# Kernel tuning notes

Hardware: AMD Instinct MI355X
Metric: run time of the kernel (lower is better)

Reference implementation:

```python
import jax, jax.numpy as jnp
import numpy as np
import math

N_HEAD = 4
NORM_GROUPS = 32
EPS = 1e-5


def setup_inputs() -> dict:
    key = jax.random.key(0)
    ks = jax.random.split(key, 6)
    C = 256
    x = jax.random.normal(ks[0], (2, C, 64, 64), dtype=jnp.float32)
    gn_w = jnp.ones((C,), dtype=jnp.float32)
    gn_b = jnp.zeros((C,), dtype=jnp.float32)
    s = 1.0 / math.sqrt(C)
    wq = jax.random.normal(ks[1], (C, C), dtype=jnp.float32) * s
    wk = jax.random.normal(ks[2], (C, C), dtype=jnp.float32) * s
    wv = jax.random.normal(ks[3], (C, C), dtype=jnp.float32) * s
    wo = jax.random.normal(ks[4], (C, C), dtype=jnp.float32) * s
    bo = jnp.zeros((C,), dtype=jnp.float32)
    return {"x": x, "gn_w": gn_w, "gn_b": gn_b, "wq": wq, "wk": wk,
            "wv": wv, "wo": wo, "bo": bo}


def group_norm(x, w, b):
    bsz, c, h, wd = x.shape
    xg = x.reshape(bsz, NORM_GROUPS, c // NORM_GROUPS, h, wd)
    mu = jnp.mean(xg, axis=(2, 3, 4), keepdims=True)
    var = jnp.mean(jnp.square(xg - mu), axis=(2, 3, 4), keepdims=True)
    xn = ((xg - mu) * jax.lax.rsqrt(var + EPS)).reshape(bsz, c, h, wd)
    return xn * w[None, :, None, None] + b[None, :, None, None]


def conv1x1(x, w):
    # w: (out_ch, in_ch) applied pointwise
    return jnp.einsum('bchw,oc->bohw', x, w)


def reference(x, gn_w, gn_b, wq, wk, wv, wo, bo):
    bsz, c, h, w = x.shape
    hd = c // N_HEAD
    norm = group_norm(x, gn_w, gn_b)
    q = conv1x1(norm, wq).reshape(bsz, N_HEAD, hd, h, w)
    k = conv1x1(norm, wk).reshape(bsz, N_HEAD, hd, h, w)
    v = conv1x1(norm, wv).reshape(bsz, N_HEAD, hd, h, w)
    # scores over full spatial positions; NOTE: scaled by sqrt(channel), as in source
    scores = jnp.einsum('bnchw,bncxy->bnhwxy', q, k) / jnp.sqrt(jnp.float32(c))
    probs = jax.nn.softmax(scores.reshape(bsz, N_HEAD, h, w, h * w), axis=-1)
    probs = probs.reshape(bsz, N_HEAD, h, w, h, w)
    out = jnp.einsum('bnhwxy,bncxy->bnchw', probs, v).reshape(bsz, c, h, w)
    out = conv1x1(out, wo) + bo[None, :, None, None]
    return out + x
```

## Files before the change

### kernel.cpp

```cpp
#include <hip/hip_runtime.h>

typedef float f32x4 __attribute__((ext_vector_type(4)));
typedef float f32x16 __attribute__((ext_vector_type(16)));
typedef short bf16x8 __attribute__((ext_vector_type(8)));
typedef unsigned short u16;
typedef unsigned int u32;
typedef unsigned int u32x2 __attribute__((ext_vector_type(2)));

#define MFMA(a, b, c) __builtin_amdgcn_mfma_f32_16x16x32_bf16((a), (b), (c), 0, 0, 0)
#define MFMA32(a, b, c) __builtin_amdgcn_mfma_f32_32x32x16_bf16((a), (b), (c), 0, 0, 0)

static __device__ __forceinline__ u16 f2bf(float f) {
    union { float f; u32 u; } v; v.f = f;
    u32 r = v.u + 0x7FFFu + ((v.u >> 16) & 1u);
    return (u16)(r >> 16);
}

static __device__ __forceinline__ u32 pkbf(float a, float b) {
    u32 ua = __float_as_uint(a) + 0x8000u;
    u32 ub = __float_as_uint(b) + 0x8000u;
    return __builtin_amdgcn_perm(ub, ua, 0x07060302);
}

static __device__ __forceinline__ void gll16(const u16* g, u16* l) {
    __builtin_amdgcn_global_load_lds(
        (const __attribute__((address_space(1))) u32*)(const void*)g,
        (__attribute__((address_space(3))) u32*)(void*)l, 16, 0, 0);
}

#define BAR_VM() do { \
    asm volatile("s_waitcnt vmcnt(0)" ::: "memory"); \
    __builtin_amdgcn_s_barrier(); \
    asm volatile("" ::: "memory"); \
} while (0)

#define BAR_LGKM() do { \
    asm volatile("s_waitcnt lgkmcnt(0)" ::: "memory"); \
    __builtin_amdgcn_s_barrier(); \
} while (0)

__global__ __launch_bounds__(256) void prep_kernel(
    const float* __restrict__ wq, const float* __restrict__ wk,
    const float* __restrict__ wv, const float* __restrict__ wo,
    const float* __restrict__ x, u16* __restrict__ Wbf,
    float2* __restrict__ part) {
    int blk = blockIdx.x;
    int t = threadIdx.x;
    if (blk < 256) {
        int base = (blk * 256 + t) * 4;
        int p = base >> 16;
        int off = base & 65535;
        const float* W = (p == 0) ? wq : ((p == 1) ? wk : ((p == 2) ? wv : wo));
        float sc = (p == 0) ? 0.09014009048f : 1.0f;
        float4 v = *(const float4*)(W + off);
        uint2 pk;
        pk.x = pkbf(v.x * sc, v.y * sc);
        pk.y = pkbf(v.z * sc, v.w * sc);
        *(uint2*)(Wbf + base) = pk;
        return;
    }
    int sblk = blk - 256;
    int bg = sblk >> 2, quarter = sblk & 3;
    const float* xp = x + (size_t)bg * 32768 + quarter * 8192;

    float s = 0.f, ss = 0.f;
#pragma unroll
    for (int rep = 0; rep < 8; ++rep) {
        float4 v = *(const float4*)(xp + t * 4 + rep * 1024);
        s += v.x + v.y + v.z + v.w;
        ss += v.x * v.x + v.y * v.y + v.z * v.z + v.w * v.w;
    }
    for (int off = 1; off < 64; off <<= 1) {
        s += __shfl_xor(s, off);
        ss += __shfl_xor(ss, off);
    }
    __shared__ float red[8];
    int lane = t & 63, w = t >> 6;
    if (lane == 0) { red[w] = s; red[4 + w] = ss; }
    __syncthreads();
    if (t == 0) {
        part[sblk] = make_float2(red[0] + red[1] + red[2] + red[3],
                                 red[4] + red[5] + red[6] + red[7]);
    }
}

__global__ __launch_bounds__(256) void qkv_gemm(
    const float* __restrict__ x, const float* __restrict__ gw,
    const float* __restrict__ gb, const float2* __restrict__ part,
    const u16* __restrict__ Wbf,
    u16* __restrict__ Q, u16* __restrict__ K, u16* __restrict__ V) {
    int b = blockIdx.y & 1;
    int p = blockIdx.y >> 1;
    const u16* W = Wbf + p * 65536;
    int bx = blockIdx.x;
    int m0 = ((bx >> 3) & 1) * 128;
    int n0 = ((bx & 7) | ((bx >> 4) << 3)) * 64;

    __shared__ u16 a_s[2][128 * 40];
    __shared__ u16 b_s[2][64 * 40];
    __shared__ float wgt_s[256], bia_s[256];

    int t = threadIdx.x;
    int lane = t & 63, wave = t >> 6;
    int wm = wave & 1, wn = wave >> 1;
    int r = lane & 15, qd = lane >> 4;

    {
        int c = t;
        int g = c >> 3;
        float s = 0.f, ss = 0.f;
#pragma unroll
        for (int q = 0; q < 4; ++q) {
            float2 pp = part[(b * 32 + g) * 4 + q];
            s += pp.x; ss += pp.y;
        }
        float mu = s * (1.f / 32768.f);
        float var = ss * (1.f / 32768.f) - mu * mu;
        float rstd = rsqrtf(var + 1e-5f);
        float wg = gw[c] * rstd;
        wgt_s[c] = wg;
        bia_s[c] = gb[c] - mu * wg;
    }
    __syncthreads();

    f32x4 acc[4][2];
#pragma unroll
    for (int i = 0; i < 4; ++i)
#pragma unroll
        for (int j = 0; j < 2; ++j) acc[i][j] = (f32x4){0.f, 0.f, 0.f, 0.f};

    int srow = t >> 1;
    int scp = (t & 1) * 16;
    int bn = t & 63;
    int bw = t >> 6;
    int bswz = ((bn >> 3) & 3) ^ (((bn >> 5) & 1) << 1);
    int bgp = ((bw ^ bswz) << 3);

    uint4 pa0, pa1;
    float pxv[8];
    auto load_regs = [&](int kk) {
        const u16* src = W + (m0 + srow) * 256 + kk + scp;
        pa0 = *(const uint4*)(src);
        pa1 = *(const uint4*)(src + 8);
        const float* xcol = x + (size_t)(b * 256 + kk + bw * 8) * 4096 + n0 + bn;
#pragma unroll
        for (int j = 0; j < 8; ++j) pxv[j] = xcol[(size_t)j * 4096];
    };
    auto write_buf = [&](int bsel, int kk) {
        *(uint4*)(a_s[bsel] + srow * 40 + scp) = pa0;
        *(uint4*)(a_s[bsel] + srow * 40 + scp + 8) = pa1;
        u32* dst = (u32*)(b_s[bsel] + bn * 40 + bgp);
#pragma unroll
        for (int j = 0; j < 4; ++j) {
            int c = kk + bw * 8 + 2 * j;
            dst[j] = pkbf(pxv[2 * j] * wgt_s[c] + bia_s[c],
                          pxv[2 * j + 1] * wgt_s[c + 1] + bia_s[c + 1]);
        }
    };

    load_regs(0);
    write_buf(0, 0);
    BAR_LGKM();

    for (int it = 0; it < 8; ++it) {
        int cur = it & 1;
        bool more = (it + 1) < 8;
        if (more) load_regs((it + 1) * 32);

        bf16x8 af[4], bf[2];
#pragma unroll
        for (int mt = 0; mt < 4; ++mt)
            af[mt] = *(const bf16x8*)(a_s[cur] + (wm * 64 + mt * 16 + r) * 40 + qd * 8);
#pragma unroll
        for (int nt = 0; nt < 2; ++nt) {
            int row = wn * 32 + nt * 16 + r;
            int rswz = ((row >> 3) & 3) ^ (((row >> 5) & 1) << 1);
            bf[nt] = *(const bf16x8*)(b_s[cur] + row * 40 + ((qd ^ rswz) << 3));
        }
        if (p == 2) {
#pragma unroll
            for (int mt = 0; mt < 4; ++mt)
#pragma unroll
                for (int nt = 0; nt < 2; ++nt)
                    acc[mt][nt] = MFMA(bf[nt], af[mt], acc[mt][nt]);
        } else {
#pragma unroll
            for (int mt = 0; mt < 4; ++mt)
#pragma unroll
                for (int nt = 0; nt < 2; ++nt)
                    acc[mt][nt] = MFMA(af[mt], bf[nt], acc[mt][nt]);
        }

        if (more) write_buf(cur ^ 1, (it + 1) * 32);
        BAR_LGKM();
    }

    if (p < 2) {
        u16* dst = (p == 0) ? Q : K;
#pragma unroll
        for (int mt = 0; mt < 4; ++mt) {
#pragma unroll
            for (int nt = 0; nt < 2; ++nt) {
                int o0 = m0 + wm * 64 + mt * 16 + qd * 4;
                int s = n0 + wn * 32 + nt * 16 + r;
                int h = o0 >> 6, d0 = o0 & 63;
                uint2 pk;
                pk.x = pkbf(acc[mt][nt][0], acc[mt][nt][1]);
                pk.y = pkbf(acc[mt][nt][2], acc[mt][nt][3]);
                *(uint2*)(dst + ((size_t)((b * 4 + h) * 4096 + s)) * 64 + d0) = pk;
            }
        }
    } else {
#pragma unroll
        for (int mt = 0; mt < 4; ++mt) {
#pragma unroll
            for (int nt = 0; nt < 2; ++nt) {
                int o = m0 + wm * 64 + mt * 16 + r;
                int h = o >> 6, d = o & 63;
                int sb = n0 + wn * 32 + nt * 16 + qd * 4;
                uint2 pk;
                pk.x = pkbf(acc[mt][nt][0], acc[mt][nt][1]);
                pk.y = pkbf(acc[mt][nt][2], acc[mt][nt][3]);
                *(uint2*)(V + ((size_t)((b * 4 + h) * 64 + d)) * 4096 + sb) = pk;
            }
        }
    }
}

template <int QT>
__global__ __launch_bounds__(256, QT == 1 ? 4 : 2) void attn_kernel(
    const u16* __restrict__ Q, const u16* __restrict__ K,
    const u16* __restrict__ V, u16* __restrict__ Opart,
    float* __restrict__ Lpart, int nk32) {
    int bh = blockIdx.x & 7, sp = blockIdx.x >> 3;
    int qb = blockIdx.y;
    int t = threadIdx.x, lane = t & 63, w = t >> 6;
    int qn = lane & 31, h = lane >> 5;

    const size_t bhoff = (size_t)bh * 4096 * 64;
    int q0 = (qb * 4 + w) * (32 * QT);
    int kbase = sp * nk32 * 32;

    __shared__ u16 smem[16384];

    bf16x8 qf[4];
#pragma unroll
    for (int c = 0; c < 4; ++c)
        qf[c] = *(const bf16x8*)(Q + bhoff +
            (size_t)(q0 + qn) * 64 + c * 16 + h * 8);

    f32x16 oacc[2];
#pragma unroll
    for (int dt = 0; dt < 2; ++dt)
#pragma unroll
        for (int i = 0; i < 16; ++i) oacc[dt][i] = 0.f;
    float lacc = 0.f;

    const u16* Kp = K + bhoff;
    const u16* Vp = V + bhoff;

    int gs = (lane & 7) ^ (lane >> 3);
    int rbase = (w & 1) * 32 + (lane >> 3);

    auto fill = [&](int bufsel, int kp) {
        u16* ld = smem + bufsel * 8192 + w * 2048;
        if (w < 2) {
            const u16* s = Kp + (size_t)(kp + rbase) * 64 + gs * 8;
#pragma unroll
            for (int j = 0; j < 4; ++j) gll16(s + j * 512, ld + j * 512);
        } else {
            const u16* s = Vp + (size_t)rbase * 4096 + kp + gs * 8;
#pragma unroll
            for (int j = 0; j < 4; ++j) gll16(s + j * 32768, ld + j * 512);
        }
    };

    int sw = qn & 7;
    auto qk = [&](const u16* buf, int j, f32x16& s) {
        bf16x8 kf[4];
        int kr = j * 32 + qn;
#pragma unroll
        for (int c = 0; c < 4; ++c)
            kf[c] = *(const bf16x8*)(buf + kr * 64 + (((c * 2 + h) ^ sw) << 3));
#pragma unroll
        for (int i = 0; i < 16; ++i) s[i] = 0.f;
        __builtin_amdgcn_s_setprio(1);
#pragma unroll
        for (int c = 0; c < 4; ++c) s = MFMA32(kf[c], qf[c], s);
        __builtin_amdgcn_s_setprio(0);
    };
    auto sm_pv = [&](const u16* buf, int j, const f32x16& s) {
        bf16x8 vf[2][2];
#pragma unroll
        for (int dt = 0; dt < 2; ++dt) {
            int d = dt * 32 + qn;
#pragma unroll
            for (int kc = 0; kc < 2; ++kc) {
                int g = j * 4 + kc * 2 + h;
                vf[dt][kc] = *(const bf16x8*)(buf + 4096 + d * 64 + ((g ^ sw) << 3));
            }
        }
        float e[16];
#pragma unroll
        for (int i = 0; i < 16; ++i)
            e[i] = __builtin_amdgcn_exp2f(s[i]);
        float t0 = (e[0] + e[1]) + (e[2] + e[3]);
        float t1 = (e[4] + e[5]) + (e[6] + e[7]);
        float t2 = (e[8] + e[9]) + (e[10] + e[11]);
        float t3 = (e[12] + e[13]) + (e[14] + e[15]);
        lacc += (t0 + t1) + (t2 + t3);

        u32 p[8];
#pragma unroll
        for (int i = 0; i < 8; ++i) p[i] = pkbf(e[2 * i], e[2 * i + 1]);

        u32x2 r0 = __builtin_amdgcn_permlane32_swap(p[0], p[2], false, false);
        u32x2 r1 = __builtin_amdgcn_permlane32_swap(p[1], p[3], false, false);
        u32x2 r2 = __builtin_amdgcn_permlane32_swap(p[4], p[6], false, false);
        u32x2 r3 = __builtin_amdgcn_permlane32_swap(p[5], p[7], false, false);
        uint4 pau = {r0[0], r1[0], r0[1], r1[1]};
        uint4 pbu = {r2[0], r3[0], r2[1], r3[1]};
        bf16x8 pA = *(const bf16x8*)&pau;
        bf16x8 pB = *(const bf16x8*)&pbu;

        __builtin_amdgcn_s_setprio(1);
#pragma unroll
        for (int dt = 0; dt < 2; ++dt) {
            oacc[dt] = MFMA32(vf[dt][0], pA, oacc[dt]);
            oacc[dt] = MFMA32(vf[dt][1], pB, oacc[dt]);
        }
        __builtin_amdgcn_s_setprio(0);
    };

    int npair = nk32 >> 1;
    fill(0, kbase);
    if (npair > 1) fill(1, kbase + 64);
    BAR_VM();

    for (int i = 0; i < npair; ++i) {
        const u16* cur = smem + (i & 1) * 8192;
        f32x16 sA, sB;
        qk(cur, 0, sA);
        qk(cur, 1, sB);
        sm_pv(cur, 0, sA);
        sm_pv(cur, 1, sB);
        BAR_VM();
        if (i + 2 < npair) fill(i & 1, kbase + (i + 2) * 64);
    }

    float lfull = lacc + __shfl_xor(lacc, 32);

    u16* my = smem + w * (32 * 72);
    size_t obase = ((size_t)sp * 8 + bh) * 4096 + q0;
#pragma unroll
    for (int dt = 0; dt < 2; ++dt) {
#pragma unroll
        for (int g = 0; g < 4; ++g) {
            int d0 = g * 8 + h * 4 + dt * 32;
            uint2 pk;
            pk.x = pkbf(oacc[dt][4 * g], oacc[dt][4 * g + 1]);
            pk.y = pkbf(oacc[dt][4 * g + 2], oacc[dt][4 * g + 3]);
            *(uint2*)(my + qn * 72 + d0) = pk;
        }
    }
#pragma unroll
    for (int rr = 0; rr < 4; ++rr) {
        int row = rr * 8 + (lane >> 3), ch = lane & 7;
        uint4 v = *(const uint4*)(my + row * 72 + ch * 8);
        *(uint4*)(Opart + (obase + row) * 64 + ch * 8) = v;
    }
    if (h == 0) Lpart[obase + qn] = lfull;
}

__global__ __launch_bounds__(256) void attn_combine(
    const u16* __restrict__ Opart, const float* __restrict__ Lpart,
    u16* __restrict__ attnT, int nsplit) {
    int t = threadIdx.x;
    int gr = blockIdx.x * 64 + (t >> 2);
    int d0 = (t & 3) * 16;

    float l = 0.f;
    for (int s = 0; s < nsplit; ++s) l += Lpart[(size_t)s * 32768 + gr];
    float inv = 1.f / l;

    float acc[16];
#pragma unroll
    for (int i = 0; i < 16; ++i) acc[i] = 0.f;
    for (int s = 0; s < nsplit; ++s) {
        const u16* p = Opart + ((size_t)s * 32768 + gr) * 64 + d0;
        uint4 a = *(const uint4*)(p);
        uint4 bq = *(const uint4*)(p + 8);
        const u32* ap = (const u32*)&a;
        const u32* bp = (const u32*)&bq;
#pragma unroll
        for (int j = 0; j < 4; ++j) {
            acc[2 * j]     += __uint_as_float(ap[j] << 16);
            acc[2 * j + 1] += __uint_as_float(ap[j] & 0xFFFF0000u);
            acc[8 + 2 * j]     += __uint_as_float(bp[j] << 16);
            acc[8 + 2 * j + 1] += __uint_as_float(bp[j] & 0xFFFF0000u);
        }
    }
    u32 pk[8];
#pragma unroll
    for (int j = 0; j < 8; ++j)
        pk[j] = pkbf(acc[2 * j] * inv, acc[2 * j + 1] * inv);

    int bh = gr >> 12, q = gr & 4095;
    int b = bh >> 2, hh = bh & 3;
    u16* dst = attnT + ((size_t)(b * 4096 + q)) * 256 + hh * 64 + d0;
    *(uint4*)(dst) = make_uint4(pk[0], pk[1], pk[2], pk[3]);
    *(uint4*)(dst + 8) = make_uint4(pk[4], pk[5], pk[6], pk[7]);
}

__global__ __launch_bounds__(256) void out_gemm(
    const u16* __restrict__ attnT, const u16* __restrict__ W3,
    const float* __restrict__ bo, const float* __restrict__ x,
    float* __restrict__ out) {
    int b = blockIdx.y;
    int bx = blockIdx.x;
    int m0 = ((bx >> 3) & 3) * 64;
    int n0 = ((bx & 7) | ((bx >> 5) << 3)) * 64;

    __shared__ u16 a_s[2][64 * 40];
    __shared__ u16 b_s[2][64 * 40];

    int t = threadIdx.x;
    int lane = t & 63, wave = t >> 6;
    int wm = wave & 1, wn = wave >> 1;
    int r = lane & 15, qd = lane >> 4;

    const u16* Bsrc = attnT + (size_t)b * 4096 * 256;

    f32x4 acc[2][2];
#pragma unroll
    for (int i = 0; i < 2; ++i)
#pragma unroll
        for (int j = 0; j < 2; ++j) acc[i][j] = (f32x4){0.f, 0.f, 0.f, 0.f};

    int u = t & 127;
    int srow = u >> 1;
    int scp = (u & 1) * 16;

    uint4 p0, p1;
    auto load_regs = [&](int kk) {
        const u16* src = (t < 128)
            ? W3 + (m0 + srow) * 256 + kk + scp
            : Bsrc + (size_t)(n0 + srow) * 256 + kk + scp;
        p0 = *(const uint4*)(src);
        p1 = *(const uint4*)(src + 8);
    };
    auto write_buf = [&](int bsel) {
        u16* dst = (t < 128) ? (a_s[bsel] + srow * 40 + scp)
                             : (b_s[bsel] + srow * 40 + scp);
        *(uint4*)(dst) = p0;
        *(uint4*)(dst + 8) = p1;
    };

    load_regs(0);
    write_buf(0);
    BAR_LGKM();

    for (int it = 0; it < 8; ++it) {
        int cur = it & 1;
        bool more = (it + 1) < 8;
        if (more) load_regs((it + 1) * 32);

        bf16x8 af[2], bf[2];
#pragma unroll
        for (int mt = 0; mt < 2; ++mt)
            af[mt] = *(const bf16x8*)(a_s[cur] + (wm * 32 + mt * 16 + r) * 40 + qd * 8);
#pragma unroll
        for (int nt = 0; nt < 2; ++nt)
            bf[nt] = *(const bf16x8*)(b_s[cur] + (wn * 32 + nt * 16 + r) * 40 + qd * 8);
#pragma unroll
        for (int mt = 0; mt < 2; ++mt)
#pragma unroll
            for (int nt = 0; nt < 2; ++nt)
                acc[mt][nt] = MFMA(af[mt], bf[nt], acc[mt][nt]);

        if (more) write_buf(cur ^ 1);
        BAR_LGKM();
    }

#pragma unroll
    for (int mt = 0; mt < 2; ++mt) {
#pragma unroll
        for (int nt = 0; nt < 2; ++nt) {
#pragma unroll
            for (int j = 0; j < 4; ++j) {
                int o = m0 + wm * 32 + mt * 16 + qd * 4 + j;
                int s = n0 + wn * 32 + nt * 16 + r;
                size_t idx = (size_t)(b * 256 + o) * 4096 + s;
                out[idx] = acc[mt][nt][j] + bo[o] + x[idx];
            }
        }
    }
}

extern "C" void kernel_launch(void* const* d_in, const int* in_sizes, int n_in,
                              void* d_out, int out_size, void* d_ws, size_t ws_size,
                              hipStream_t stream) {
    const float* x = (const float*)d_in[0];
    const float* gn_w = (const float*)d_in[1];
    const float* gn_b = (const float*)d_in[2];
    const float* wq = (const float*)d_in[3];
    const float* wk = (const float*)d_in[4];
    const float* wv = (const float*)d_in[5];
    const float* wo = (const float*)d_in[6];
    const float* bo = (const float*)d_in[7];
    float* out = (float*)d_out;

    char* ws = (char*)d_ws;
    u16* attnT = (u16*)(ws);
    u16* Q     = (u16*)(ws + (4u << 20));
    u16* Kp    = (u16*)(ws + (8u << 20));
    u16* Vp    = (u16*)(ws + (12u << 20));
    u16* Wbf   = (u16*)(ws + (16u << 20));
    float2* part = (float2*)(ws + (16u << 20) + 524288);

    size_t opart_off = (size_t)17 << 20;
    size_t osplit = 8ull * 4096 * 64 * 2;
    int nsplit = (ws_size >= opart_off + 4 * osplit + 4ull * 32768 * 4 + 4096) ? 4 : 2;
    u16* Opart = (u16*)(ws + opart_off);
    float* Lpart = (float*)(ws + opart_off + (size_t)nsplit * osplit);

    prep_kernel<<<512, 256, 0, stream>>>(wq, wk, wv, wo, x, Wbf, part);
    qkv_gemm<<<dim3(128, 6), 256, 0, stream>>>(x, gn_w, gn_b, part, Wbf, Q, Kp, Vp);
    attn_kernel<1><<<dim3(8 * nsplit, 32), 256, 0, stream>>>(
        Q, Kp, Vp, Opart, Lpart, 128 / nsplit);
    attn_combine<<<512, 256, 0, stream>>>(Opart, Lpart, attnT, nsplit);
    out_gemm<<<dim3(256, 2), 256, 0, stream>>>(attnT, Wbf + 3 * 65536, bo, x, out);
}
```

Before: 139.9 us.

## Fuse Q, K, V projections into one block sharing normalized x tile

The QKV GEMM now computes all three projections in each block for a 64-row output tile, so the group-normalized, bf16-converted x tile is loaded and converted once instead of three times. This cuts global reads of x and the repeated normalization math across the three separate projection launches. In exchange each block holds three accumulator sets and a larger A-tile shared buffer, and the grid shrinks to 512 blocks, which may change occupancy and register pressure.

```diff
diff --git a/kernel.cpp b/kernel.cpp
--- a/kernel.cpp
+++ b/kernel.cpp
@@ -89,14 +89,12 @@
     const float* __restrict__ gb, const float2* __restrict__ part,
     const u16* __restrict__ Wbf,
     u16* __restrict__ Q, u16* __restrict__ K, u16* __restrict__ V) {
-    int b = blockIdx.y & 1;
-    int p = blockIdx.y >> 1;
-    const u16* W = Wbf + p * 65536;
+    int b = blockIdx.y;
     int bx = blockIdx.x;
-    int m0 = ((bx >> 3) & 1) * 128;
-    int n0 = ((bx & 7) | ((bx >> 4) << 3)) * 64;
-
-    __shared__ u16 a_s[2][128 * 40];
+    int m0 = ((bx >> 3) & 3) * 64;
+    int n0 = ((bx & 7) | ((bx >> 5) << 3)) * 64;
+
+    __shared__ u16 a_s[2][3][64 * 40];
     __shared__ u16 b_s[2][64 * 40];
     __shared__ float wgt_s[256], bia_s[256];
 
@@ -123,32 +121,35 @@
     }
     __syncthreads();
 
-    f32x4 acc[4][2];
-#pragma unroll
-    for (int i = 0; i < 4; ++i)
-#pragma unroll
-        for (int j = 0; j < 2; ++j) acc[i][j] = (f32x4){0.f, 0.f, 0.f, 0.f};
-
-    int srow = t >> 1;
-    int scp = (t & 1) * 16;
+    f32x4 acc[3][2][2];
+#pragma unroll
+    for (int p = 0; p < 3; ++p)
+#pragma unroll
+        for (int i = 0; i < 2; ++i)
+#pragma unroll
+            for (int j = 0; j < 2; ++j) acc[p][i][j] = (f32x4){0.f, 0.f, 0.f, 0.f};
+
+    int ar = t >> 2;
+    int ac = (t & 3) * 8;
     int bn = t & 63;
     int bw = t >> 6;
     int bswz = ((bn >> 3) & 3) ^ (((bn >> 5) & 1) << 1);
     int bgp = ((bw ^ bswz) << 3);
 
-    uint4 pa0, pa1;
+    uint4 pa[3];
     float pxv[8];
     auto load_regs = [&](int kk) {
-        const u16* src = W + (m0 + srow) * 256 + kk + scp;
-        pa0 = *(const uint4*)(src);
-        pa1 = *(const uint4*)(src + 8);
+#pragma unroll
+        for (int p = 0; p < 3; ++p)
+            pa[p] = *(const uint4*)(Wbf + p * 65536 + (m0 + ar) * 256 + kk + ac);
         const float* xcol = x + (size_t)(b * 256 + kk + bw * 8) * 4096 + n0 + bn;
 #pragma unroll
         for (int j = 0; j < 8; ++j) pxv[j] = xcol[(size_t)j * 4096];
     };
     auto write_buf = [&](int bsel, int kk) {
-        *(uint4*)(a_s[bsel] + srow * 40 + scp) = pa0;
-        *(uint4*)(a_s[bsel] + srow * 40 + scp + 8) = pa1;
+#pragma unroll
+        for (int p = 0; p < 3; ++p)
+            *(uint4*)(a_s[bsel][p] + ar * 40 + ac) = pa[p];
         u32* dst = (u32*)(b_s[bsel] + bn * 40 + bgp);
 #pragma unroll
         for (int j = 0; j < 4; ++j) {
@@ -167,62 +168,60 @@
         bool more = (it + 1) < 8;
         if (more) load_regs((it + 1) * 32);
 
-        bf16x8 af[4], bf[2];
-#pragma unroll
-        for (int mt = 0; mt < 4; ++mt)
-            af[mt] = *(const bf16x8*)(a_s[cur] + (wm * 64 + mt * 16 + r) * 40 + qd * 8);
+        bf16x8 af[3][2], bf[2];
+#pragma unroll
+        for (int p = 0; p < 3; ++p)
+#pragma unroll
+            for (int mt = 0; mt < 2; ++mt)
+                af[p][mt] = *(const bf16x8*)(a_s[cur][p] +
+                    (wm * 32 + mt * 16 + r) * 40 + qd * 8);
 #pragma unroll
         for (int nt = 0; nt < 2; ++nt) {
             int row = wn * 32 + nt * 16 + r;
             int rswz = ((row >> 3) & 3) ^ (((row >> 5) & 1) << 1);
             bf[nt] = *(const bf16x8*)(b_s[cur] + row * 40 + ((qd ^ rswz) << 3));
         }
-        if (p == 2) {
-#pragma unroll
-            for (int mt = 0; mt < 4; ++mt)
-#pragma unroll
-                for (int nt = 0; nt < 2; ++nt)
-                    acc[mt][nt] = MFMA(bf[nt], af[mt], acc[mt][nt]);
-        } else {
-#pragma unroll
-            for (int mt = 0; mt < 4; ++mt)
-#pragma unroll
-                for (int nt = 0; nt < 2; ++nt)
-                    acc[mt][nt] = MFMA(af[mt], bf[nt], acc[mt][nt]);
-        }
+#pragma unroll
+        for (int mt = 0; mt < 2; ++mt)
+#pragma unroll
+            for (int nt = 0; nt < 2; ++nt) {
+                acc[0][mt][nt] = MFMA(af[0][mt], bf[nt], acc[0][mt][nt]);
+                acc[1][mt][nt] = MFMA(af[1][mt], bf[nt], acc[1][mt][nt]);
+                acc[2][mt][nt] = MFMA(bf[nt], af[2][mt], acc[2][mt][nt]);
+            }
 
         if (more) write_buf(cur ^ 1, (it + 1) * 32);
         BAR_LGKM();
     }
 
-    if (p < 2) {
+#pragma unroll
+    for (int p = 0; p < 2; ++p) {
         u16* dst = (p == 0) ? Q : K;
 #pragma unroll
-        for (int mt = 0; mt < 4; ++mt) {
+        for (int mt = 0; mt < 2; ++mt) {
 #pragma unroll
             for (int nt = 0; nt < 2; ++nt) {
-                int o0 = m0 + wm * 64 + mt * 16 + qd * 4;
+                int o0 = m0 + wm * 32 + mt * 16 + qd * 4;
                 int s = n0 + wn * 32 + nt * 16 + r;
                 int h = o0 >> 6, d0 = o0 & 63;
                 uint2 pk;
-                pk.x = pkbf(acc[mt][nt][0], acc[mt][nt][1]);
-                pk.y = pkbf(acc[mt][nt][2], acc[mt][nt][3]);
+                pk.x = pkbf(acc[p][mt][nt][0], acc[p][mt][nt][1]);
+                pk.y = pkbf(acc[p][mt][nt][2], acc[p][mt][nt][3]);
                 *(uint2*)(dst + ((size_t)((b * 4 + h) * 4096 + s)) * 64 + d0) = pk;
             }
         }
-    } else {
-#pragma unroll
-        for (int mt = 0; mt < 4; ++mt) {
-#pragma unroll
-            for (int nt = 0; nt < 2; ++nt) {
-                int o = m0 + wm * 64 + mt * 16 + r;
-                int h = o >> 6, d = o & 63;
-                int sb = n0 + wn * 32 + nt * 16 + qd * 4;
-                uint2 pk;
-                pk.x = pkbf(acc[mt][nt][0], acc[mt][nt][1]);
-                pk.y = pkbf(acc[mt][nt][2], acc[mt][nt][3]);
-                *(uint2*)(V + ((size_t)((b * 4 + h) * 64 + d)) * 4096 + sb) = pk;
-            }
+    }
+#pragma unroll
+    for (int mt = 0; mt < 2; ++mt) {
+#pragma unroll
+        for (int nt = 0; nt < 2; ++nt) {
+            int o = m0 + wm * 32 + mt * 16 + r;
+            int h = o >> 6, d = o & 63;
+            int sb = n0 + wn * 32 + nt * 16 + qd * 4;
+            uint2 pk;
+            pk.x = pkbf(acc[2][mt][nt][0], acc[2][mt][nt][1]);
+            pk.y = pkbf(acc[2][mt][nt][2], acc[2][mt][nt][3]);
+            *(uint2*)(V + ((size_t)((b * 4 + h) * 64 + d)) * 4096 + sb) = pk;
         }
     }
 }
@@ -525,7 +524,7 @@
     float* Lpart = (float*)(ws + opart_off + (size_t)nsplit * osplit);
 
     prep_kernel<<<512, 256, 0, stream>>>(wq, wk, wv, wo, x, Wbf, part);
-    qkv_gemm<<<dim3(128, 6), 256, 0, stream>>>(x, gn_w, gn_b, part, Wbf, Q, Kp, Vp);
+    qkv_gemm<<<dim3(256, 2), 256, 0, stream>>>(x, gn_w, gn_b, part, Wbf, Q, Kp, Vp);
     attn_kernel<1><<<dim3(8 * nsplit, 32), 256, 0, stream>>>(
         Q, Kp, Vp, Opart, Lpart, 128 / nsplit);
     attn_combine<<<512, 256, 0, stream>>>(Opart, Lpart, attnT, nsplit);
```

After: 148.1 us. 1.06x slower.
